# Performance work log

Measured on AMD Instinct MI355X. Metric: run time of the kernel, lower is better.

## Reference

```python
import jax, jax.numpy as jnp
import numpy as np

N_ANCHORS = 3
N_CLASSES = 1
N_CH = 5 + N_CLASSES  # x,y,w,h,obj,cls
FSIZE = 64
STRIDE = 8
CONF_THRE = 0.01
NMS_THRE = 0.45
ANCHORS = np.array([[10.0, 13.0], [16.0, 30.0], [33.0, 23.0]], dtype=np.float32)


def setup_inputs() -> dict:
    key = jax.random.key(0)
    feat = jax.random.normal(key, (1, N_ANCHORS * N_CH, FSIZE, FSIZE), dtype=jnp.float32)
    anchors = jnp.asarray(ANCHORS)
    return {"feat": feat, "anchors": anchors}


def _decode(feat, anchors):
    # feat: [B, A*C, F, F] -> [B, A, F, F, C] (matches view+permute in torch code)
    B, _, F, _ = feat.shape
    out = feat.reshape(B, N_ANCHORS, N_CH, F, F).transpose(0, 1, 3, 4, 2)
    xy = jax.nn.sigmoid(out[..., 0:2])          # sigmoid on x,y
    conf = jax.nn.sigmoid(out[..., 4:])         # sigmoid on obj + classes
    grid = jnp.arange(F, dtype=feat.dtype)
    x = xy[..., 0] + grid[None, None, None, :]  # x varies along W
    y = xy[..., 1] + grid[None, None, :, None]  # y varies along H
    aw = (anchors[:, 0] / STRIDE)[None, :, None, None]
    ah = (anchors[:, 1] / STRIDE)[None, :, None, None]
    w = jnp.exp(out[..., 2]) * aw
    h = jnp.exp(out[..., 3]) * ah
    boxes = jnp.stack([x, y, w, h], axis=-1) * STRIDE  # grid units -> pixels
    return jnp.concatenate([boxes, conf], axis=-1).reshape(B, -1, N_CH)  # [B, N, 6]


def _greedy_nms(boxes_xyxy, scores, valid, thresh):
    # boxes sorted by score desc, then sequential greedy suppression
    N = boxes_xyxy.shape[0]
    order = jnp.argsort(-scores)
    b = boxes_xyxy[order]
    v = valid[order]
    area = (b[:, 2] - b[:, 0]) * (b[:, 3] - b[:, 1])
    tl = jnp.maximum(b[:, None, :2], b[None, :, :2])   # [N, N, 2]
    br = jnp.minimum(b[:, None, 2:], b[None, :, 2:])
    inter = jnp.prod(br - tl, axis=-1) * jnp.all(tl < br, axis=-1)
    iou = inter / (area[:, None] + area[None, :] - inter)
    idx = jnp.arange(N)

    def body(keep, inp):
        row, i, vi = inp
        suppressed = jnp.any((row >= thresh) & keep & (idx < i))
        k = vi & jnp.logical_not(suppressed)
        return keep.at[i].set(k), None

    keep_sorted, _ = jax.lax.scan(body, jnp.zeros(N, dtype=bool), (iou, idx, v))
    return jnp.zeros(N, dtype=bool).at[order].set(keep_sorted)  # back to input order


def reference(feat, anchors):
    pred = _decode(feat, anchors)  # [1, N, 6] = cx,cy,w,h,obj,cls
    p = pred[0]
    # center form -> corner form (postprocess box_corner step)
    x1 = p[:, 0] - p[:, 2] / 2
    y1 = p[:, 1] - p[:, 3] / 2
    x2 = p[:, 0] + p[:, 2] / 2
    y2 = p[:, 1] + p[:, 3] / 2
    obj = p[:, 4]
    cls_conf = jnp.max(p[:, 5:5 + N_CLASSES], axis=1)  # single class
    score = obj * cls_conf
    valid = score >= CONF_THRE
    boxes = jnp.stack([x1, y1, x2, y2], axis=1)
    keep = _greedy_nms(boxes, score, valid, NMS_THRE)
    det = jnp.concatenate([boxes, obj[:, None], cls_conf[:, None]], axis=1)
    det = det * keep.astype(det.dtype)[:, None]  # suppressed boxes zeroed (fixed shape)
    return det[None], keep[None]
```

## Files before the change

### kernel.cpp

```cpp
#include <hip/hip_runtime.h>
#include <stdint.h>

#define NTOT   12288
#define NW     192
#define NCH    6
#define ECAP   1500000
#define CONF_THR 0.01f

typedef unsigned long long u64;
typedef uint32_t u32;

__device__ __forceinline__ float sigmf(float x){ return 1.0f/(1.0f+expf(-x)); }

__device__ __forceinline__ bool sup_exact(float4 a, float aar, float4 b, float bar){
  float tlx=fmaxf(a.x,b.x), tly=fmaxf(a.y,b.y);
  float brx=fminf(a.z,b.z), bry=fminf(a.w,b.w);
  float inter = __fmul_rn(__fsub_rn(brx,tlx), __fsub_rn(bry,tly));
  float d     = __fsub_rn(__fadd_rn(aar,bar), inter);
  bool ov = (tlx<brx) && (tly<bry);
  const double M = 30198987.0/67108864.0;
  return ov && ((double)inter >= M*(double)d);
}

__global__ void k_decode(const float* __restrict__ feat, const float* __restrict__ anchors,
                         float4* __restrict__ obox, float* __restrict__ oobj,
                         float* __restrict__ ocls, float* __restrict__ oscore,
                         u32* __restrict__ okey, int* __restrict__ rank,
                         u64* __restrict__ validw, u32* __restrict__ ecnt){
  int n = blockIdx.x*256 + threadIdx.x;
  if(blockIdx.x==0){
    if(threadIdx.x<NW) validw[threadIdx.x]=0ull;
    if(threadIdx.x==NW) *ecnt=0u;
  }
  int a = n >> 12;
  int cell = n & 4095;
  int gy = cell >> 6, gx = cell & 63;
  const float* f = feat + a*NCH*4096 + cell;
  float v0=f[0], v1=f[4096], v2=f[8192], v3=f[12288], v4=f[16384], v5=f[20480];
  float aw = anchors[2*a]   * 0.125f;
  float ah = anchors[2*a+1] * 0.125f;
  float px = (sigmf(v0) + (float)gx) * 8.0f;
  float py = (sigmf(v1) + (float)gy) * 8.0f;
  float pw = (expf(v2)*aw) * 8.0f;
  float ph = (expf(v3)*ah) * 8.0f;
  float obj = sigmf(v4), cls = sigmf(v5);
  float4 b;
  b.x = px - pw*0.5f; b.y = py - ph*0.5f;
  b.z = px + pw*0.5f; b.w = py + ph*0.5f;
  float sc = obj*cls;
  obox[n]=b; oobj[n]=obj; ocls[n]=cls; oscore[n]=sc;
  u32 u = __float_as_uint(sc);
  u32 asc = (u & 0x80000000u) ? ~u : (u | 0x80000000u);
  okey[n] = ~asc;
  rank[n] = 0;
}

__global__ __launch_bounds__(256) void k_rank_part(const u32* __restrict__ okey,
                                                   int* __restrict__ rank){
  __shared__ u32 tile[1024];
  int n = blockIdx.x*256 + threadIdx.x;
  int t0 = blockIdx.y * 1024;
  u32 my = okey[n];
  for(int k=threadIdx.x;k<1024;k+=256) tile[k]=okey[t0+k];
  __syncthreads();
  int r0=0,r1=0,r2=0,r3=0;
  #pragma unroll 4
  for(int k=0;k<1024;k+=4){
    uint4 kj = *reinterpret_cast<const uint4*>(&tile[k]);
    int j = t0+k;
    r0 += (int)((kj.x<my)||(kj.x==my && (j  )<n));
    r1 += (int)((kj.y<my)||(kj.y==my && (j+1)<n));
    r2 += (int)((kj.z<my)||(kj.z==my && (j+2)<n));
    r3 += (int)((kj.w<my)||(kj.w==my && (j+3)<n));
  }
  atomicAdd(&rank[n], r0+r1+r2+r3);
}

__global__ void k_scatter(const int* __restrict__ rank,
                          const float4* __restrict__ obox,const float* __restrict__ oobj,
                          const float* __restrict__ ocls,const float* __restrict__ oscore,
                          float4* __restrict__ sbox,float* __restrict__ sarea,
                          float* __restrict__ sobj,float* __restrict__ scls,
                          int* __restrict__ order,u64* __restrict__ validw){
  int n = blockIdx.x*256 + threadIdx.x;
  int r = rank[n];
  float4 b = obox[n];
  sbox[r]=b;
  sarea[r]=(b.z-b.x)*(b.w-b.y);
  sobj[r]=oobj[n]; scls[r]=ocls[n];
  order[r]=n;
  if(oscore[n] >= CONF_THR)
    atomicOr(&validw[r>>6], 1ull<<(unsigned)(r&63));
}

__global__ __launch_bounds__(256) void k_cols(
    const float4* __restrict__ sbox, const float* __restrict__ sarea,
    const u64* __restrict__ validw_g,
    uint4* __restrict__ entries, uint2* __restrict__ boxOff, u32* __restrict__ ecnt)
{
  __shared__ uint4 stg[4][2][NW];
  __shared__ u64 vwL[NW];
  int tid=threadIdx.x, lane=tid&63, wvl=tid>>6;
  for(int t=tid;t<NW;t+=256) vwL[t]=validw_g[t];
  __syncthreads();
  int g  = blockIdx.x*4 + wvl;
  int j1 = g, j2 = NTOT-1-g;
  bool val1 = (vwL[j1>>6]>>(unsigned)(j1&63))&1ull;
  bool val2 = (vwL[j2>>6]>>(unsigned)(j2&63))&1ull;
  float4 b1=sbox[j1], b2=sbox[j2];
  float ar1=sarea[j1], ar2=sarea[j2];
  int B1=j1>>6, B2=j2>>6;
  u32 cnt1=0, cnt2=0;
  int vend = val2 ? B2 : (val1 ? B1 : -1);
  #pragma unroll 1
  for(int v=0; v<=vend; ++v){
    int i = (v<<6)|lane;
    float4 a = sbox[i];
    float ai = sarea[i];
    u64 vw = vwL[v];
    if(val2){
      bool s2 = (i<j2) && sup_exact(a,ai,b2,ar2);
      u64 w2 = __ballot(s2) & vw;
      if(w2){ if(lane==0) stg[wvl][1][cnt2]=make_uint4((u32)v,(u32)w2,(u32)(w2>>32),0u); cnt2++; }
    }
    if(val1 && v<=B1){
      bool s1 = (i<j1) && sup_exact(a,ai,b1,ar1);
      u64 w1 = __ballot(s1) & vw;
      if(w1){ if(lane==0) stg[wvl][0][cnt1]=make_uint4((u32)v,(u32)w1,(u32)(w1>>32),0u); cnt1++; }
    }
  }
  u32 tot = cnt1+cnt2, base=0;
  if(lane==0 && tot) base = atomicAdd(ecnt, tot);
  base = (u32)__builtin_amdgcn_readfirstlane((int)base);
  if(lane==0){
    boxOff[j1]=make_uint2(base,      cnt1);
    boxOff[j2]=make_uint2(base+cnt1, cnt2);
  }
  asm volatile("s_waitcnt lgkmcnt(0)" ::: "memory");
  for(u32 e=lane;e<cnt1;e+=64) if(base+e<ECAP)      entries[base+e]     =stg[wvl][0][e];
  for(u32 e=lane;e<cnt2;e+=64) if(base+cnt1+e<ECAP) entries[base+cnt1+e]=stg[wvl][1][e];
}

__global__ __launch_bounds__(1024) void k_gs(
    const u64* __restrict__ validw_g, const uint2* __restrict__ boxOff,
    const uint4* __restrict__ entries, u64* __restrict__ keepw_g)
{
  __shared__ u64 kcur[NW], validL[NW];
  __shared__ u32 chg[2];
  int tid=threadIdx.x, lane=tid&63, wv=tid>>6;
  for(int t=tid;t<NW;t+=1024){ u64 v=validw_g[t]; validL[t]=v; kcur[t]=v; }
  if(tid<2) chg[tid]=0u;
  uint2 off[12];
  #pragma unroll
  for(int k=0;k<12;k++) off[k]=boxOff[((wv*12+k)<<6)|lane];
  __syncthreads();
  for(int r=0;;++r){
    int f=r&1;
    if(tid==0) chg[f^1]=0u;
    bool any=false;
    #pragma unroll 1
    for(int k=0;k<12;k++){
      int w = wv*12+k;
      u64 valw = validL[w];
      u64 old  = kcur[w];
      bool bv = (valw>>(unsigned)lane)&1ull;
      u32 base=off[k].x, cnt = bv ? off[k].y : 0u;
      bool killed=false;
      for(u32 e=0;e<cnt;e++){
        uint4 en = entries[base+e];
        if(kcur[en.x] & ((((u64)en.z)<<32)|(u64)en.y)){ killed=true; break; }
      }
      u64 nk = valw & ~__ballot(killed);
      if(nk != old){ any=true; if(lane==0) kcur[w]=nk; }
      asm volatile("s_waitcnt lgkmcnt(0)" ::: "memory");
    }
    if(any && lane==0) chg[f]=1u;
    __syncthreads();
    u32 c = chg[f];
    __syncthreads();
    if(!c) break;
  }
  for(int t=tid;t<NW;t+=1024) keepw_g[t]=kcur[t];
}

__global__ void k_final(const int* __restrict__ order,const u64* __restrict__ keepw,
                        const float4* __restrict__ sbox,const float* __restrict__ sobj,
                        const float* __restrict__ scls,float* __restrict__ out){
  int i = blockIdx.x*256 + threadIdx.x;
  int n = order[i];
  u64 kw = keepw[i>>6];
  float kf = ((kw>>(unsigned)(i&63))&1ull) ? 1.0f : 0.0f;
  float4 b = sbox[i];
  float* det = out + (size_t)n*6;
  det[0]=b.x*kf; det[1]=b.y*kf; det[2]=b.z*kf; det[3]=b.w*kf;
  det[4]=sobj[i]*kf; det[5]=scls[i]*kf;
  out[NTOT*6 + n] = kf;
}

extern "C" void kernel_launch(void* const* d_in,const int* in_sizes,int n_in,
                              void* d_out,int out_size,void* d_ws,size_t ws_size,
                              hipStream_t stream){
  const float* feat=(const float*)d_in[0];
  const float* anchors=(const float*)d_in[1];
  float* out=(float*)d_out;

  char* w=(char*)d_ws;
  auto alloc=[&](size_t bytes)->char*{ char* p=w; w += (bytes+255)&~255ull; return p; };
  float4 *obox =(float4*)alloc(NTOT*16);
  float  *oobj =(float*) alloc(NTOT*4);
  float  *ocls =(float*) alloc(NTOT*4);
  float  *oscore=(float*)alloc(NTOT*4);
  u32    *okey =(u32*)   alloc(NTOT*4);
  int    *rank =(int*)   alloc(NTOT*4);
  float4 *sbox =(float4*)alloc(NTOT*16);
  float  *sarea=(float*) alloc(NTOT*4);
  float  *sobj =(float*) alloc(NTOT*4);
  float  *scls =(float*) alloc(NTOT*4);
  int    *order=(int*)   alloc(NTOT*4);
  u64    *validw =(u64*) alloc(NW*8);
  u64    *keepw  =(u64*) alloc(NW*8);
  u32    *ecnt   =(u32*) alloc(256);
  uint2  *boxOff =(uint2*)alloc((size_t)NTOT*8);
  uint4  *entries=(uint4*)alloc((size_t)ECAP*16);

  hipLaunchKernelGGL(k_decode, dim3(NTOT/256),dim3(256),0,stream,
                     feat,anchors,obox,oobj,ocls,oscore,okey,rank,validw,ecnt);
  hipLaunchKernelGGL(k_rank_part, dim3(NTOT/256,12),dim3(256),0,stream, okey,rank);
  hipLaunchKernelGGL(k_scatter, dim3(NTOT/256),dim3(256),0,stream,
                     rank,obox,oobj,ocls,oscore,sbox,sarea,sobj,scls,order,validw);
  hipLaunchKernelGGL(k_cols, dim3(NTOT/8),dim3(256),0,stream,
                     sbox,sarea,validw,entries,boxOff,ecnt);
  hipLaunchKernelGGL(k_gs, dim3(1),dim3(1024),0,stream,
                     validw,boxOff,entries,keepw);
  hipLaunchKernelGGL(k_final, dim3(NTOT/256),dim3(256),0,stream,
                     order,keepw,sbox,sobj,scls,out);
}
```

Baseline: 179.1 us.

## Process four columns per wave in k_cols with shared row-box loads

Each wave now handles four column boxes (two balanced pairs) instead of two, so every row-box load from sbox is reused across four IoU tests. The row loop is unrolled by two, box areas are recomputed on the fly instead of being stored in a separate sarea array, and the grid is halved. Staging buffers are capped at 48 entries per column, with a recompute fallback that writes directly to global memory when a column overflows. This trades more registers and lower wave count for less global-load traffic and fewer launched waves.

```diff
diff --git a/kernel.cpp b/kernel.cpp
--- a/kernel.cpp
+++ b/kernel.cpp
@@ -5,6 +5,7 @@
 #define NW     192
 #define NCH    6
 #define ECAP   1500000
+#define CAP    48
 #define CONF_THR 0.01f
 
 typedef unsigned long long u64;
@@ -79,14 +80,12 @@
 __global__ void k_scatter(const int* __restrict__ rank,
                           const float4* __restrict__ obox,const float* __restrict__ oobj,
                           const float* __restrict__ ocls,const float* __restrict__ oscore,
-                          float4* __restrict__ sbox,float* __restrict__ sarea,
+                          float4* __restrict__ sbox,
                           float* __restrict__ sobj,float* __restrict__ scls,
                           int* __restrict__ order,u64* __restrict__ validw){
   int n = blockIdx.x*256 + threadIdx.x;
   int r = rank[n];
-  float4 b = obox[n];
-  sbox[r]=b;
-  sarea[r]=(b.z-b.x)*(b.w-b.y);
+  sbox[r]=obox[n];
   sobj[r]=oobj[n]; scls[r]=ocls[n];
   order[r]=n;
   if(oscore[n] >= CONF_THR)
@@ -94,51 +93,79 @@
 }
 
 __global__ __launch_bounds__(256) void k_cols(
-    const float4* __restrict__ sbox, const float* __restrict__ sarea,
-    const u64* __restrict__ validw_g,
+    const float4* __restrict__ sbox, const u64* __restrict__ validw_g,
     uint4* __restrict__ entries, uint2* __restrict__ boxOff, u32* __restrict__ ecnt)
 {
-  __shared__ uint4 stg[4][2][NW];
+  __shared__ uint4 stg[4][4][CAP];
   __shared__ u64 vwL[NW];
   int tid=threadIdx.x, lane=tid&63, wvl=tid>>6;
   for(int t=tid;t<NW;t+=256) vwL[t]=validw_g[t];
   __syncthreads();
-  int g  = blockIdx.x*4 + wvl;
-  int j1 = g, j2 = NTOT-1-g;
-  bool val1 = (vwL[j1>>6]>>(unsigned)(j1&63))&1ull;
-  bool val2 = (vwL[j2>>6]>>(unsigned)(j2&63))&1ull;
-  float4 b1=sbox[j1], b2=sbox[j2];
-  float ar1=sarea[j1], ar2=sarea[j2];
-  int B1=j1>>6, B2=j2>>6;
-  u32 cnt1=0, cnt2=0;
-  int vend = val2 ? B2 : (val1 ? B1 : -1);
-  #pragma unroll 1
-  for(int v=0; v<=vend; ++v){
-    int i = (v<<6)|lane;
-    float4 a = sbox[i];
-    float ai = sarea[i];
-    u64 vw = vwL[v];
-    if(val2){
-      bool s2 = (i<j2) && sup_exact(a,ai,b2,ar2);
-      u64 w2 = __ballot(s2) & vw;
-      if(w2){ if(lane==0) stg[wvl][1][cnt2]=make_uint4((u32)v,(u32)w2,(u32)(w2>>32),0u); cnt2++; }
-    }
-    if(val1 && v<=B1){
-      bool s1 = (i<j1) && sup_exact(a,ai,b1,ar1);
-      u64 w1 = __ballot(s1) & vw;
-      if(w1){ if(lane==0) stg[wvl][0][cnt1]=make_uint4((u32)v,(u32)w1,(u32)(w1>>32),0u); cnt1++; }
-    }
-  }
-  u32 tot = cnt1+cnt2, base=0;
-  if(lane==0 && tot) base = atomicAdd(ecnt, tot);
-  base = (u32)__builtin_amdgcn_readfirstlane((int)base);
-  if(lane==0){
-    boxOff[j1]=make_uint2(base,      cnt1);
-    boxOff[j2]=make_uint2(base+cnt1, cnt2);
-  }
+  int g = blockIdx.x*4 + wvl;
+  int jq[4] = {g, 6143-g, 6144+g, 12287-g};
+  float4 bj[4]; float arj[4]; bool val[4]; int Bj[4]; u32 cnt[4]={0,0,0,0};
+  int vend=-1;
+  #pragma unroll
+  for(int q=0;q<4;q++){
+    int j=jq[q];
+    bj[q]=sbox[j];
+    arj[q]=(bj[q].z-bj[q].x)*(bj[q].w-bj[q].y);
+    val[q]=(vwL[j>>6]>>(unsigned)(j&63))&1ull;
+    Bj[q]=j>>6;
+    if(val[q]) vend=Bj[q];
+  }
+  int v=0;
+  for(; v+1<=vend; v+=2){
+    int i0=(v<<6)|lane, i1=i0+64;
+    float4 a0=sbox[i0], a1=sbox[i1];
+    float ai0=(a0.z-a0.x)*(a0.w-a0.y);
+    float ai1=(a1.z-a1.x)*(a1.w-a1.y);
+    u64 vw0=vwL[v], vw1=vwL[v+1];
+    #pragma unroll
+    for(int q=0;q<4;q++){
+      bool s0 = val[q] && (v   <=Bj[q]) && (i0<jq[q]) && sup_exact(a0,ai0,bj[q],arj[q]);
+      bool s1 = val[q] && (v+1 <=Bj[q]) && (i1<jq[q]) && sup_exact(a1,ai1,bj[q],arj[q]);
+      u64 w0=__ballot(s0)&vw0;
+      u64 w1=__ballot(s1)&vw1;
+      if(w0){ if(lane==0 && cnt[q]<CAP) stg[wvl][q][cnt[q]]=make_uint4((u32)v,  (u32)w0,(u32)(w0>>32),0u); cnt[q]++; }
+      if(w1){ if(lane==0 && cnt[q]<CAP) stg[wvl][q][cnt[q]]=make_uint4((u32)(v+1),(u32)w1,(u32)(w1>>32),0u); cnt[q]++; }
+    }
+  }
+  if(v<=vend){
+    int i0=(v<<6)|lane;
+    float4 a0=sbox[i0];
+    float ai0=(a0.z-a0.x)*(a0.w-a0.y);
+    u64 vw0=vwL[v];
+    #pragma unroll
+    for(int q=0;q<4;q++){
+      bool s0 = val[q] && (v<=Bj[q]) && (i0<jq[q]) && sup_exact(a0,ai0,bj[q],arj[q]);
+      u64 w0=__ballot(s0)&vw0;
+      if(w0){ if(lane==0 && cnt[q]<CAP) stg[wvl][q][cnt[q]]=make_uint4((u32)v,(u32)w0,(u32)(w0>>32),0u); cnt[q]++; }
+    }
+  }
+  u32 tot=cnt[0]+cnt[1]+cnt[2]+cnt[3], base=0;
+  if(lane==0 && tot) base=atomicAdd(ecnt,tot);
+  base=(u32)__builtin_amdgcn_readfirstlane((int)base);
   asm volatile("s_waitcnt lgkmcnt(0)" ::: "memory");
-  for(u32 e=lane;e<cnt1;e+=64) if(base+e<ECAP)      entries[base+e]     =stg[wvl][0][e];
-  for(u32 e=lane;e<cnt2;e+=64) if(base+cnt1+e<ECAP) entries[base+cnt1+e]=stg[wvl][1][e];
+  u32 off=base;
+  #pragma unroll
+  for(int q=0;q<4;q++){
+    if(lane==0) boxOff[jq[q]]=make_uint2(off,cnt[q]);
+    if(cnt[q]<=CAP){
+      for(u32 e=lane;e<cnt[q];e+=64) if(off+e<ECAP) entries[off+e]=stg[wvl][q][e];
+    } else {
+      u32 pos=0;
+      for(int vv=0; vv<=Bj[q]; ++vv){
+        int i=(vv<<6)|lane;
+        float4 a=sbox[i];
+        float ai=(a.z-a.x)*(a.w-a.y);
+        bool s=(i<jq[q])&&sup_exact(a,ai,bj[q],arj[q]);
+        u64 wb=__ballot(s)&vwL[vv];
+        if(wb){ if(lane==0 && off+pos<ECAP) entries[off+pos]=make_uint4((u32)vv,(u32)wb,(u32)(wb>>32),0u); pos++; }
+      }
+    }
+    off+=cnt[q];
+  }
 }
 
 __global__ __launch_bounds__(1024) void k_gs(
@@ -213,7 +240,6 @@
   u32    *okey =(u32*)   alloc(NTOT*4);
   int    *rank =(int*)   alloc(NTOT*4);
   float4 *sbox =(float4*)alloc(NTOT*16);
-  float  *sarea=(float*) alloc(NTOT*4);
   float  *sobj =(float*) alloc(NTOT*4);
   float  *scls =(float*) alloc(NTOT*4);
   int    *order=(int*)   alloc(NTOT*4);
@@ -227,9 +253,9 @@
                      feat,anchors,obox,oobj,ocls,oscore,okey,rank,validw,ecnt);
   hipLaunchKernelGGL(k_rank_part, dim3(NTOT/256,12),dim3(256),0,stream, okey,rank);
   hipLaunchKernelGGL(k_scatter, dim3(NTOT/256),dim3(256),0,stream,
-                     rank,obox,oobj,ocls,oscore,sbox,sarea,sobj,scls,order,validw);
-  hipLaunchKernelGGL(k_cols, dim3(NTOT/8),dim3(256),0,stream,
-                     sbox,sarea,validw,entries,boxOff,ecnt);
+                     rank,obox,oobj,ocls,oscore,sbox,sobj,scls,order,validw);
+  hipLaunchKernelGGL(k_cols, dim3(NTOT/16),dim3(256),0,stream,
+                     sbox,validw,entries,boxOff,ecnt);
   hipLaunchKernelGGL(k_gs, dim3(1),dim3(1024),0,stream,
                      validw,boxOff,entries,keepw);
   hipLaunchKernelGGL(k_final, dim3(NTOT/256),dim3(256),0,stream,
```

New measurement: 184.1 us. 1.03x slower.
